# Kernel optimization log

Measured on AMD Instinct MI355X. Metric: run time of the kernel, lower is better.

## Reference

```python
import jax, jax.numpy as jnp
import numpy as np

EMBED_DIM = 1024
HIDDEN = 4 * EMBED_DIM
BATCH, SEQ = 4, 4096
EPS = 1e-5


def setup_inputs() -> dict:
    key = jax.random.key(0)
    k1, k2, k3 = jax.random.split(key, 3)
    x = jax.random.normal(k1, (BATCH, SEQ, EMBED_DIM), dtype=jnp.float32)
    # Kaiming-ish init scale for linear weights
    w1 = jax.random.normal(k2, (HIDDEN, EMBED_DIM), dtype=jnp.float32) * (1.0 / np.sqrt(EMBED_DIM))
    w2 = jax.random.normal(k3, (EMBED_DIM, HIDDEN), dtype=jnp.float32) * (1.0 / np.sqrt(HIDDEN))
    return {"x": x, "w1": w1, "w2": w2}


def _quant_weight(w):
    # BitNet-b1.58 absmean ternary quantization: clip(round(w/s), -1, 1) * s
    s = jnp.clip(jnp.mean(jnp.abs(w)), EPS, None)
    wq = jnp.clip(jnp.round(w / s), -1.0, 1.0) * s
    # straight-through estimator
    return w + jax.lax.stop_gradient(wq - w)


def _quant_act(x):
    # int8 per-token absmax quantization of activations
    scale = 127.0 / jnp.clip(jnp.max(jnp.abs(x), axis=-1, keepdims=True), EPS, None)
    xq = jnp.clip(jnp.round(x * scale), -128.0, 127.0) / scale
    return x + jax.lax.stop_gradient(xq - x)


def _bitlinear(x, w):
    # x: [..., in], w: [out, in] -> [..., out]
    return jnp.einsum('bsi,oi->bso', _quant_act(x), _quant_weight(w))


def reference(x, w1, w2):
    h = jax.nn.gelu(_bitlinear(x, w1), approximate=False)  # nn.GELU default = exact erf
    return _bitlinear(h, w2)  # dropout is identity in eval / p=0
```

## Files before the change

kernel.cpp:

```cpp
#include <hip/hip_runtime.h>
#include <hip/hip_bf16.h>
#include <cstdint>
#include <cmath>

typedef int intx4 __attribute__((ext_vector_type(4)));

#define EPSQ 1e-5f

__device__ __forceinline__ void async16(const void* g, void* l) {
  __builtin_amdgcn_global_load_lds(
      (const __attribute__((address_space(1))) unsigned int*)(uintptr_t)g,
      (__attribute__((address_space(3))) unsigned int*)(unsigned int)(uintptr_t)l,
      16, 0, 0);
}

__device__ __forceinline__ int q8(float v, float scale, float lo, float hi) {
  return (int)fminf(fmaxf(rintf(v * scale), lo), hi);
}

__device__ __forceinline__ float fast_gelu(float y) {
  const float t = y * 0.70710678118654752f;
  const float x = fabsf(t);
  const float u = __builtin_amdgcn_rcpf(__builtin_fmaf(0.3275911f, x, 1.0f));
  float p = __builtin_fmaf(1.061405429f, u, -1.453152027f);
  p = __builtin_fmaf(p, u, 1.421413741f);
  p = __builtin_fmaf(p, u, -0.284496736f);
  p = __builtin_fmaf(p, u, 0.254829592f);
  p = p * u;
  const float e = __expf(-x * x);
  const float erf_abs = __builtin_fmaf(-p, e, 1.0f);
  const float erf_t = copysignf(erf_abs, t);
  return 0.5f * y * (1.0f + erf_t);
}

__global__ void k_init(float* rowmax, double* sums) {
  int i = blockIdx.x * 256 + threadIdx.x;
  if (i < 16384) rowmax[i] = 0.0f;
  if (i < 2) sums[i] = 0.0;
}

__global__ __launch_bounds__(256) void k_absmean2(const float* __restrict__ W1,
                                                  const float* __restrict__ W2,
                                                  double* __restrict__ sums) {
  __shared__ double wsum[4];
  const int tid = threadIdx.x;
  const int which = blockIdx.x >> 11;
  const float* __restrict__ W = which ? W2 : W1;
  const size_t base = ((size_t)(blockIdx.x & 2047) * 256 + tid) * 8;
  float4 a = *(const float4*)(W + base);
  float4 b = *(const float4*)(W + base + 4);
  float s = fabsf(a.x) + fabsf(a.y) + fabsf(a.z) + fabsf(a.w) +
            fabsf(b.x) + fabsf(b.y) + fabsf(b.z) + fabsf(b.w);
  double d = (double)s;
#pragma unroll
  for (int i = 1; i < 64; i <<= 1) d += __shfl_xor(d, i);
  const int lane = tid & 63, wave = tid >> 6;
  if (lane == 0) wsum[wave] = d;
  __syncthreads();
  if (tid == 0) atomicAdd(sums + which, wsum[0] + wsum[1] + wsum[2] + wsum[3]);
}

__global__ __launch_bounds__(256) void k_quantw2(const float* __restrict__ W1,
                                                 const float* __restrict__ W2,
                                                 signed char* __restrict__ W1Q,
                                                 signed char* __restrict__ W2Q,
                                                 const double* __restrict__ sums) {
  const int which = blockIdx.x >> 11;
  const float* __restrict__ W = which ? W2 : W1;
  signed char* __restrict__ WQ = which ? W2Q : W1Q;
  const float s = fmaxf((float)(sums[which] * (1.0 / 4194304.0)), EPSQ);
  const float inv_s = 1.0f / s;
  const size_t base = ((size_t)(blockIdx.x & 2047) * 256 + threadIdx.x) * 8;
  float4 a = *(const float4*)(W + base);
  float4 b = *(const float4*)(W + base + 4);
  float v[8] = {a.x, a.y, a.z, a.w, b.x, b.y, b.z, b.w};
  unsigned int lo = 0, hi = 0;
#pragma unroll
  for (int j = 0; j < 4; ++j) {
    lo |= ((unsigned int)(q8(v[j], inv_s, -1.f, 1.f) & 0xff)) << (8 * j);
    hi |= ((unsigned int)(q8(v[4 + j], inv_s, -1.f, 1.f) & 0xff)) << (8 * j);
  }
  uint2 o; o.x = lo; o.y = hi;
  *(uint2*)(WQ + base) = o;
}

__global__ __launch_bounds__(256) void k_quantx(const float* __restrict__ X,
                                                signed char* __restrict__ XQ,
                                                float* __restrict__ dqx) {
  __shared__ float wmax[4];
  const int row = blockIdx.x, tid = threadIdx.x;
  const size_t base = (size_t)row * 1024 + tid * 4;
  float4 a = *(const float4*)(X + base);
  float m = fmaxf(fmaxf(fabsf(a.x), fabsf(a.y)), fmaxf(fabsf(a.z), fabsf(a.w)));
#pragma unroll
  for (int i = 1; i < 64; i <<= 1) m = fmaxf(m, __shfl_xor(m, i));
  const int lane = tid & 63, wave = tid >> 6;
  if (lane == 0) wmax[wave] = m;
  __syncthreads();
  m = fmaxf(fmaxf(wmax[0], wmax[1]), fmaxf(wmax[2], wmax[3]));
  m = fmaxf(m, EPSQ);
  const float scale = 127.f / m;
  if (tid == 0) dqx[row] = m * (1.f / 127.f);
  unsigned int p = ((unsigned int)(q8(a.x, scale, -128.f, 127.f) & 0xff)) |
                   ((unsigned int)(q8(a.y, scale, -128.f, 127.f) & 0xff) << 8) |
                   ((unsigned int)(q8(a.z, scale, -128.f, 127.f) & 0xff) << 16) |
                   ((unsigned int)(q8(a.w, scale, -128.f, 127.f) & 0xff) << 24);
  *(unsigned int*)(XQ + base) = p;
}

template <int KB>
__device__ __forceinline__ void gemm_mainloop(const signed char* __restrict__ A,
                                              const signed char* __restrict__ B,
                                              int bm, int bn, int tid, char* lds,
                                              intx4 (&acc)[4][4]) {
  const int wave = tid >> 6, lane = tid & 63;
  const int wm = wave >> 1, wn = wave & 1;
  const int kq = lane >> 4, lc = lane & 15;

  size_t ag[4], bg[4];
#pragma unroll
  for (int i = 0; i < 4; ++i) {
    int gidx = i * 256 + tid;
    int r = gidx >> 3, g = gidx & 7;
    int gs = g ^ (r & 7);
    ag[i] = (size_t)(bm * 128 + r) * KB + gs * 16;
    bg[i] = (size_t)(bn * 128 + r) * KB + gs * 16;
  }
  int aoff[2][4], boff[2][4];
#pragma unroll
  for (int ks = 0; ks < 2; ++ks) {
#pragma unroll
    for (int t = 0; t < 4; ++t) {
      int ra = wm * 64 + t * 16 + lc;
      aoff[ks][t] = ra * 128 + (((ks * 4 + kq) ^ (ra & 7)) << 4);
      int rb = wn * 64 + t * 16 + lc;
      boff[ks][t] = 16384 + rb * 128 + (((ks * 4 + kq) ^ (rb & 7)) << 4);
    }
  }
#pragma unroll
  for (int ti = 0; ti < 4; ++ti)
#pragma unroll
    for (int tj = 0; tj < 4; ++tj) {
      intx4 z = {0, 0, 0, 0};
      acc[ti][tj] = z;
    }

  for (int kt = 0; kt < KB / 128; ++kt) {
    __syncthreads();
    const int k0 = kt * 128;
#pragma unroll
    for (int i = 0; i < 4; ++i) {
      async16(A + ag[i] + k0, lds + i * 4096 + wave * 1024);
      async16(B + bg[i] + k0, lds + 16384 + i * 4096 + wave * 1024);
    }
    asm volatile("s_waitcnt vmcnt(0)" ::: "memory");
    __syncthreads();
#pragma unroll
    for (int ks = 0; ks < 2; ++ks) {
      intx4 af[4], bfr[4];
#pragma unroll
      for (int t = 0; t < 4; ++t) af[t] = *(const intx4*)(lds + aoff[ks][t]);
#pragma unroll
      for (int t = 0; t < 4; ++t) bfr[t] = *(const intx4*)(lds + boff[ks][t]);
#pragma unroll
      for (int ti = 0; ti < 4; ++ti)
#pragma unroll
        for (int tj = 0; tj < 4; ++tj)
          acc[ti][tj] =
              __builtin_amdgcn_mfma_i32_16x16x64_i8(af[ti], bfr[tj], acc[ti][tj], 0, 0, 0);
    }
  }
}

__global__ __launch_bounds__(256) void k_gemm1(const signed char* __restrict__ A,
                                               const signed char* __restrict__ B,
                                               const float* __restrict__ dqx,
                                               const double* __restrict__ sums,
                                               float* __restrict__ H,
                                               float* __restrict__ rowmax) {
  __shared__ __attribute__((aligned(16))) char lds[32768];
  __shared__ float smax[128];
  const int tid = threadIdx.x;
  const int bm = blockIdx.x, bn = blockIdx.y;
  if (tid < 128) smax[tid] = 0.0f;

  intx4 acc[4][4];
  gemm_mainloop<1024>(A, B, bm, bn, tid, lds, acc);

  const int wave = tid >> 6, lane = tid & 63;
  const int wm = wave >> 1, wn = wave & 1;
  const int kq = lane >> 4, lc = lane & 15;
  const float s1 = fmaxf((float)(sums[0] * (1.0 / 4194304.0)), EPSQ);
#pragma unroll
  for (int ti = 0; ti < 4; ++ti) {
#pragma unroll
    for (int r = 0; r < 4; ++r) {
      const int lrow = wm * 64 + ti * 16 + kq * 4 + r;
      const int crow = bm * 128 + lrow;
      const float f = s1 * dqx[crow];
      float mx = 0.f;
#pragma unroll
      for (int tj = 0; tj < 4; ++tj) {
        const int gcol = bn * 128 + wn * 64 + tj * 16 + lc;
        float y = (float)acc[ti][tj][r] * f;
        float h = fast_gelu(y);
        H[(size_t)crow * 4096 + gcol] = h;
        mx = fmaxf(mx, fabsf(h));
      }
      atomicMax((unsigned int*)&smax[lrow], __float_as_uint(mx));
    }
  }
  __syncthreads();
  if (tid < 128)
    atomicMax((unsigned int*)&rowmax[bm * 128 + tid], __float_as_uint(smax[tid]));
}

__global__ __launch_bounds__(256) void k_quanth(const float* __restrict__ H,
                                                const float* __restrict__ rowmax,
                                                signed char* __restrict__ HQ) {
  const size_t gid = (size_t)blockIdx.x * 256 + threadIdx.x;
  const size_t base = gid * 4;
  const int row = (int)(base >> 12);
  const float m = fmaxf(rowmax[row], EPSQ);
  const float scale = 127.f / m;
  float4 h = *(const float4*)(H + base);
  unsigned int p = ((unsigned int)(q8(h.x, scale, -128.f, 127.f) & 0xff)) |
                   ((unsigned int)(q8(h.y, scale, -128.f, 127.f) & 0xff) << 8) |
                   ((unsigned int)(q8(h.z, scale, -128.f, 127.f) & 0xff) << 16) |
                   ((unsigned int)(q8(h.w, scale, -128.f, 127.f) & 0xff) << 24);
  *(unsigned int*)(HQ + base) = p;
}

__global__ __launch_bounds__(256) void k_gemm2(const signed char* __restrict__ A,
                                               const signed char* __restrict__ B,
                                               const float* __restrict__ rowmax,
                                               const double* __restrict__ sums,
                                               float* __restrict__ OUT) {
  __shared__ __attribute__((aligned(16))) char lds[32768];
  const int tid = threadIdx.x;
  const int bm = blockIdx.x, bn = blockIdx.y;

  intx4 acc[4][4];
  gemm_mainloop<4096>(A, B, bm, bn, tid, lds, acc);

  const int wave = tid >> 6, lane = tid & 63;
  const int wm = wave >> 1, wn = wave & 1;
  const int kq = lane >> 4, lc = lane & 15;
  const float s2 = fmaxf((float)(sums[0] * (1.0 / 4194304.0)), EPSQ);
#pragma unroll
  for (int ti = 0; ti < 4; ++ti) {
#pragma unroll
    for (int r = 0; r < 4; ++r) {
      const int crow = bm * 128 + wm * 64 + ti * 16 + kq * 4 + r;
      const float dqh = fmaxf(rowmax[crow], EPSQ) * (1.f / 127.f);
      const float f = s2 * dqh;
#pragma unroll
      for (int tj = 0; tj < 4; ++tj) {
        const int gcol = bn * 128 + wn * 64 + tj * 16 + lc;
        OUT[(size_t)crow * 1024 + gcol] = (float)acc[ti][tj][r] * f;
      }
    }
  }
}

extern "C" void kernel_launch(void* const* d_in, const int* in_sizes, int n_in,
                              void* d_out, int out_size, void* d_ws, size_t ws_size,
                              hipStream_t stream) {
  const float* X  = (const float*)d_in[0];
  const float* W1 = (const float*)d_in[1];
  const float* W2 = (const float*)d_in[2];
  float* OUT = (float*)d_out;

  char* ws = (char*)d_ws;
  signed char* W1Q = (signed char*)(ws);
  signed char* W2Q = (signed char*)(ws + (4u << 20));
  float* DQX       = (float*)(ws + (8u << 20));
  float* ROWMAX    = (float*)(ws + (8u << 20) + 65536);
  double* SUMS     = (double*)(ws + (8u << 20) + 131072);
  signed char* HQ  = (signed char*)(ws + (9u << 20));
  const size_t fixed = 73u << 20;
  float* H = (float*)(ws + fixed);

  signed char* XQ = (signed char*)((char*)d_out + 50331648ull);

  int R = 128;
  const int cands[8] = {16384, 8192, 4096, 2048, 1024, 512, 256, 128};
  for (int i = 0; i < 8; ++i) {
    if (fixed + (size_t)cands[i] * 16384ull <= ws_size) { R = cands[i]; break; }
  }

  hipLaunchKernelGGL(k_init, dim3(64), dim3(256), 0, stream, ROWMAX, SUMS);
  hipLaunchKernelGGL(k_absmean2, dim3(4096), dim3(256), 0, stream, W1, W2, SUMS);
  hipLaunchKernelGGL(k_quantw2, dim3(4096), dim3(256), 0, stream, W1, W2, W1Q, W2Q, SUMS);
  hipLaunchKernelGGL(k_quantx, dim3(16384), dim3(256), 0, stream, X, XQ, DQX);

  const int nchunk = 16384 / R;
  for (int c = 0; c < nchunk; ++c) {
    const int row0 = c * R;
    hipLaunchKernelGGL(k_gemm1, dim3(R / 128, 32), dim3(256), 0, stream,
                       XQ + (size_t)row0 * 1024, W1Q, DQX + row0, SUMS, H, ROWMAX + row0);
    hipLaunchKernelGGL(k_quanth, dim3(R * 4), dim3(256), 0, stream,
                       H, ROWMAX + row0, HQ + (size_t)row0 * 4096);
  }
  hipLaunchKernelGGL(k_gemm2, dim3(128, 8), dim3(256), 0, stream,
                     HQ, W2Q, ROWMAX, SUMS + 1, OUT);
}
```

Before: 454.4 us.

## Store GELU intermediate as block-scaled int16 instead of fp32

The first GEMM epilogue now quantizes each GELU output to int16 using a per-row, per-128-column block max, and writes that block max to a side buffer. The requantization kernel then reads the int16 values and rescales them to int8 using the block max and the global row max. This halves the intermediate traffic written and read through memory, at the cost of an extra rounding step that can shift a few int8 values relative to direct fp32 quantization. The epilogue also gains extra syncs and a second pass over the accumulators.

```diff
diff --git a/kernel.cpp b/kernel.cpp
--- a/kernel.cpp
+++ b/kernel.cpp
@@ -4,6 +4,7 @@
 #include <cmath>
 
 typedef int intx4 __attribute__((ext_vector_type(4)));
+typedef short shortx8 __attribute__((ext_vector_type(8)));
 
 #define EPSQ 1e-5f
 
@@ -176,13 +177,12 @@
                                                const signed char* __restrict__ B,
                                                const float* __restrict__ dqx,
                                                const double* __restrict__ sums,
-                                               float* __restrict__ H,
+                                               short* __restrict__ HS,
+                                               float* __restrict__ mblk,
                                                float* __restrict__ rowmax) {
   __shared__ __attribute__((aligned(16))) char lds[32768];
-  __shared__ float smax[128];
   const int tid = threadIdx.x;
   const int bm = blockIdx.x, bn = blockIdx.y;
-  if (tid < 128) smax[tid] = 0.0f;
 
   intx4 acc[4][4];
   gemm_mainloop<1024>(A, B, bm, bn, tid, lds, acc);
@@ -191,6 +191,12 @@
   const int wm = wave >> 1, wn = wave & 1;
   const int kq = lane >> 4, lc = lane & 15;
   const float s1 = fmaxf((float)(sums[0] * (1.0 / 4194304.0)), EPSQ);
+
+  __syncthreads();
+  float* smax = (float*)lds;
+  if (tid < 128) smax[tid] = 0.0f;
+  __syncthreads();
+
 #pragma unroll
   for (int ti = 0; ti < 4; ++ti) {
 #pragma unroll
@@ -201,34 +207,57 @@
       float mx = 0.f;
 #pragma unroll
       for (int tj = 0; tj < 4; ++tj) {
-        const int gcol = bn * 128 + wn * 64 + tj * 16 + lc;
         float y = (float)acc[ti][tj][r] * f;
         float h = fast_gelu(y);
-        H[(size_t)crow * 4096 + gcol] = h;
+        acc[ti][tj][r] = (int)__float_as_uint(h);
         mx = fmaxf(mx, fabsf(h));
       }
       atomicMax((unsigned int*)&smax[lrow], __float_as_uint(mx));
     }
   }
   __syncthreads();
-  if (tid < 128)
+  if (tid < 128) {
+    mblk[(size_t)(bm * 128 + tid) * 32 + bn] = smax[tid];
     atomicMax((unsigned int*)&rowmax[bm * 128 + tid], __float_as_uint(smax[tid]));
-}
-
-__global__ __launch_bounds__(256) void k_quanth(const float* __restrict__ H,
+  }
+
+#pragma unroll
+  for (int ti = 0; ti < 4; ++ti) {
+#pragma unroll
+    for (int r = 0; r < 4; ++r) {
+      const int lrow = wm * 64 + ti * 16 + kq * 4 + r;
+      const int crow = bm * 128 + lrow;
+      const float sc = 32767.0f / fmaxf(smax[lrow], 1e-30f);
+#pragma unroll
+      for (int tj = 0; tj < 4; ++tj) {
+        const int gcol = bn * 128 + wn * 64 + tj * 16 + lc;
+        float h = __uint_as_float((unsigned int)acc[ti][tj][r]);
+        int v = (int)fminf(fmaxf(rintf(h * sc), -32767.f), 32767.f);
+        HS[(size_t)crow * 4096 + gcol] = (short)v;
+      }
+    }
+  }
+}
+
+__global__ __launch_bounds__(256) void k_quanth(const short* __restrict__ HS,
+                                                const float* __restrict__ mblk,
                                                 const float* __restrict__ rowmax,
                                                 signed char* __restrict__ HQ) {
   const size_t gid = (size_t)blockIdx.x * 256 + threadIdx.x;
-  const size_t base = gid * 4;
+  const size_t base = gid * 8;
   const int row = (int)(base >> 12);
+  const int blk = (int)((base >> 7) & 31);
   const float m = fmaxf(rowmax[row], EPSQ);
-  const float scale = 127.f / m;
-  float4 h = *(const float4*)(H + base);
-  unsigned int p = ((unsigned int)(q8(h.x, scale, -128.f, 127.f) & 0xff)) |
-                   ((unsigned int)(q8(h.y, scale, -128.f, 127.f) & 0xff) << 8) |
-                   ((unsigned int)(q8(h.z, scale, -128.f, 127.f) & 0xff) << 16) |
-                   ((unsigned int)(q8(h.w, scale, -128.f, 127.f) & 0xff) << 24);
-  *(unsigned int*)(HQ + base) = p;
+  const float fb = mblk[(size_t)row * 32 + blk] * (127.0f / 32767.0f) / m;
+  shortx8 s = *(const shortx8*)(HS + base);
+  unsigned int lo = 0, hi = 0;
+#pragma unroll
+  for (int j = 0; j < 4; ++j) {
+    lo |= ((unsigned int)(q8((float)s[j], fb, -128.f, 127.f) & 0xff)) << (8 * j);
+    hi |= ((unsigned int)(q8((float)s[4 + j], fb, -128.f, 127.f) & 0xff)) << (8 * j);
+  }
+  uint2 o; o.x = lo; o.y = hi;
+  *(uint2*)(HQ + base) = o;
 }
 
 __global__ __launch_bounds__(256) void k_gemm2(const signed char* __restrict__ A,
@@ -277,16 +306,17 @@
   float* DQX       = (float*)(ws + (8u << 20));
   float* ROWMAX    = (float*)(ws + (8u << 20) + 65536);
   double* SUMS     = (double*)(ws + (8u << 20) + 131072);
-  signed char* HQ  = (signed char*)(ws + (9u << 20));
-  const size_t fixed = 73u << 20;
-  float* H = (float*)(ws + fixed);
+  float* MBLK      = (float*)(ws + (9u << 20));
+  signed char* HQ  = (signed char*)(ws + (11u << 20));
+  const size_t fixed = 75u << 20;
+  short* HS = (short*)(ws + fixed);
 
   signed char* XQ = (signed char*)((char*)d_out + 50331648ull);
 
   int R = 128;
   const int cands[8] = {16384, 8192, 4096, 2048, 1024, 512, 256, 128};
   for (int i = 0; i < 8; ++i) {
-    if (fixed + (size_t)cands[i] * 16384ull <= ws_size) { R = cands[i]; break; }
+    if (fixed + (size_t)cands[i] * 8192ull <= ws_size) { R = cands[i]; break; }
   }
 
   hipLaunchKernelGGL(k_init, dim3(64), dim3(256), 0, stream, ROWMAX, SUMS);
@@ -298,9 +328,11 @@
   for (int c = 0; c < nchunk; ++c) {
     const int row0 = c * R;
     hipLaunchKernelGGL(k_gemm1, dim3(R / 128, 32), dim3(256), 0, stream,
-                       XQ + (size_t)row0 * 1024, W1Q, DQX + row0, SUMS, H, ROWMAX + row0);
-    hipLaunchKernelGGL(k_quanth, dim3(R * 4), dim3(256), 0, stream,
-                       H, ROWMAX + row0, HQ + (size_t)row0 * 4096);
+                       XQ + (size_t)row0 * 1024, W1Q, DQX + row0, SUMS,
+                       HS, MBLK + (size_t)row0 * 32, ROWMAX + row0);
+    hipLaunchKernelGGL(k_quanth, dim3(R * 2), dim3(256), 0, stream,
+                       HS, MBLK + (size_t)row0 * 32, ROWMAX + row0,
+                       HQ + (size_t)row0 * 4096);
   }
   hipLaunchKernelGGL(k_gemm2, dim3(128, 8), dim3(256), 0, stream,
                      HQ, W2Q, ROWMAX, SUMS + 1, OUT);
```

New measurement: 452.9 us. About the same (-0.3%).
